# Optimization experiments

Hardware: AMD Instinct MI355X
Metric: run time of the kernel (lower is better)

The kernel has to match this reference:

```python
import jax, jax.numpy as jnp
import numpy as np

N_U = 50000; N_I = 50000; DIM = 64; NNZ = 2_000_000; Q = 5
LAYERS = 2; B = 1024; P = 10; NNEG = 40
MARGIN = 0.5; LAMBDA1 = 0.2; BATCH_USER = 1024


def setup_inputs() -> dict:
    key = jax.random.key(0)
    ks = jax.random.split(key, 12)
    return {
        "E_u_0": jax.random.normal(ks[0], (N_U, DIM), jnp.float32) * 0.1,
        "E_i_0": jax.random.normal(ks[1], (N_I, DIM), jnp.float32) * 0.1,
        "vals": jax.random.uniform(ks[2], (NNZ,), jnp.float32) * 0.05,  # normalized adj values
        "u_mul_s": jax.random.normal(ks[3], (N_U, Q), jnp.float32) * 0.1,
        "vt": jax.random.normal(ks[4], (Q, N_I), jnp.float32) * 0.1,
        "v_mul_s": jax.random.normal(ks[5], (N_I, Q), jnp.float32) * 0.1,
        "ut": jax.random.normal(ks[6], (Q, N_U), jnp.float32) * 0.1,
        "rows": jax.random.randint(ks[7], (NNZ,), 0, N_U, jnp.int32),
        "cols": jax.random.randint(ks[8], (NNZ,), 0, N_I, jnp.int32),
        "uids": jax.random.randint(ks[9], (B,), 0, N_U, jnp.int32),
        "pos": jax.random.randint(ks[10], (B, P), 0, N_I, jnp.int32),
        "neg": jax.random.randint(ks[11], (B, NNEG), 0, N_I, jnp.int32),
    }


def _leaky(x):
    return jnp.where(x > 0, x, 0.5 * x)  # LeakyReLU(0.5)


def reference(E_u_0, E_i_0, vals, u_mul_s, vt, v_mul_s, ut, rows, cols, uids, pos, neg):
    # --- GCN propagation (dropout=0 -> sparse_dropout is identity) ---
    E_u, E_i = E_u_0, E_i_0
    sum_u, sum_i = E_u_0, E_i_0
    for _ in range(LAYERS):
        # spmm(adj, E_i): out[r] += val * E_i[c]
        Z_du = _leaky(jax.ops.segment_sum(vals[:, None] * E_i[cols], rows, num_segments=N_U))
        # spmm(adj.T, E_u): out[c] += val * E_u[r]
        Z_di = _leaky(jax.ops.segment_sum(vals[:, None] * E_u[rows], cols, num_segments=N_I))
        # SVD hyper-conv (computed in original forward; unused by returned loss)
        G_u = _leaky(u_mul_s @ (vt @ E_i))
        G_i = _leaky(v_mul_s @ (ut @ E_u))
        del G_u, G_i
        E_u, E_i = Z_du + E_u, Z_di + E_i
        sum_u, sum_i = sum_u + E_u, sum_i + E_i

    # --- U_IConstLoss, vectorized over the original per-uid Python loop ---
    u_emb = sum_u[uids]                                  # [B, D]
    pos_emb = sum_i[pos]                                 # [B, P, D]
    neg_emb = sum_i[neg]                                 # [B, N, D]
    pos_scores = jnp.einsum("bd,bpd->bp", u_emb, pos_emb)
    neg_scores = jnp.einsum("bd,bnd->bn", u_emb, neg_emb)
    # pos_d = score at argmin == min; neg_d = score at argmax == max
    pos_d = pos_scores.min(axis=1)
    neg_d = neg_scores.max(axis=1)
    delta = jnp.where(neg_d - pos_d > 0.005, 10.0 * (pos_d - neg_d), 0.0)
    # loss_d accumulates across the loop and the running value is added each iter
    loss_d_cum = jnp.cumsum(delta)
    pos_hinge = jax.nn.relu(1.0 - pos_scores).sum(axis=1)          # sum over P
    neg_hinge = jax.nn.relu(neg_scores - MARGIN).sum(axis=1)       # scalar per user
    bpr_sum = pos_hinge + P * neg_hinge                            # bpr.sum() per user
    loss_r = (bpr_sum.sum() + loss_d_cum.sum()) / BATCH_USER
    loss = loss_r + LAMBDA1
    return loss
```

## Files before the change

### kernel.cpp

```cpp
#include <hip/hip_runtime.h>

#define N_U   50000
#define N_I   50000
#define NSEG  (N_U + N_I)
#define DIM   64
#define B_USERS 1024
#define P_POS 10
#define N_NEG 40

#define BSEG  128
#define NBUK  782
#define CAP   8192
#define EPB   4096
#define TPAD  16

#ifndef __has_builtin
#define __has_builtin(x) 0
#endif
#if __has_builtin(__builtin_amdgcn_cvt_pk_f32_fp8) && __has_builtin(__builtin_amdgcn_cvt_pk_fp8_f32)
#define HAVE_FP8 1
#else
#define HAVE_FP8 0
#endif

typedef float f32x2 __attribute__((ext_vector_type(2)));

__device__ __forceinline__ unsigned f2b(float f) {
    unsigned b = __float_as_uint(f);
    return (b + 0x7FFFu + ((b >> 16) & 1u)) >> 16;
}
__device__ __forceinline__ float b2f(unsigned u) {
    return __uint_as_float(u << 16);
}
__device__ __forceinline__ float blo(unsigned u) { return __uint_as_float(u << 16); }
__device__ __forceinline__ float bhi(unsigned u) { return __uint_as_float(u & 0xFFFF0000u); }

#if !HAVE_FP8
__device__ __forceinline__ float dec8(unsigned v) {
    unsigned s = (v >> 7) & 1u, ef = (v >> 3) & 0xFu, m = v & 7u;
    float r = (ef == 0u) ? (float)m * 0.001953125f
                         : __uint_as_float(((ef + 120u) << 23) | (m << 20));
    return s ? -r : r;
}
__device__ __forceinline__ unsigned enc8(float f) {
    unsigned b = __float_as_uint(f);
    unsigned s = b >> 31;
    float a = fabsf(f);
    if (a >= 448.f) return (s << 7) | 0x7Eu;
    if (a < 0.015625f) return s << 7;
    int e = (int)((b >> 23) & 0xFF) - 120;
    unsigned m = b & 0x7FFFFFu;
    unsigned keep = m >> 20, rem = m & 0xFFFFFu;
    keep += (rem > 0x80000u) || (rem == 0x80000u && (keep & 1u));
    if (keep == 8u) { keep = 0u; ++e; if (e > 15) return (s << 7) | 0x7Eu; }
    if (e == 15 && keep == 7u) keep = 6u;
    return (s << 7) | ((unsigned)e << 3) | keep;
}
#endif

__device__ __forceinline__ void dec4v(unsigned u, f32x2& p01, f32x2& p23) {
#if HAVE_FP8
    p01 = __builtin_amdgcn_cvt_pk_f32_fp8((int)u, false);
    p23 = __builtin_amdgcn_cvt_pk_f32_fp8((int)u, true);
#else
    p01.x = dec8(u & 0xFFu); p01.y = dec8((u >> 8) & 0xFFu);
    p23.x = dec8((u >> 16) & 0xFFu); p23.y = dec8(u >> 24);
#endif
}
__device__ __forceinline__ unsigned enc4(float f0, float f1, float f2, float f3) {
#if HAVE_FP8
    int w = 0;
    w = __builtin_amdgcn_cvt_pk_fp8_f32(f0, f1, w, false);
    w = __builtin_amdgcn_cvt_pk_fp8_f32(f2, f3, w, true);
    return (unsigned)w;
#else
    return enc8(f0) | (enc8(f1) << 8) | (enc8(f2) << 16) | (enc8(f3) << 24);
#endif
}

__device__ __forceinline__ void pkfma(f32x2& a, f32x2 b, f32x2 c) {
    asm("v_pk_fma_f32 %0, %1, %2, %0" : "+v"(a) : "v"(b), "v"(c));
}
__device__ __forceinline__ void pkadd(f32x2& a, f32x2 t) {
    asm("v_pk_add_f32 %0, %0, %1" : "+v"(a) : "v"(t));
}

__device__ __forceinline__ unsigned encv8(unsigned fbits) {
    unsigned exp8 = (fbits >> 23) & 0xFFu;
    unsigned man4 = ((fbits >> 19) & 0xFu) + ((fbits >> 18) & 1u);
    if (man4 == 16u) { man4 = 0u; exp8 += 1u; }
    int ex = (int)exp8 - 107;
    if (ex <= 0) return 0u;
    if (ex > 15) { ex = 15; man4 = 15u; }
    return ((unsigned)ex << 4) | man4;
}
__device__ __forceinline__ unsigned decv8(unsigned v8) {
    return v8 ? ((((v8 >> 4) + 107u) << 7) | ((v8 & 0xFu) << 3)) : 0u;
}

__global__ void k_conv(const float* __restrict__ Eu0, const float* __restrict__ Ei0,
                       ushort* __restrict__ E0b, unsigned* __restrict__ E0f8) {
    int p = blockIdx.x * blockDim.x + threadIdx.x;
    if (p >= NSEG * (DIM / 4)) return;
    float4 v = (p < N_U * (DIM / 4)) ? ((const float4*)Eu0)[p]
                                     : ((const float4*)Ei0)[p - N_U * (DIM / 4)];
    ushort4 o;
    o.x = (ushort)f2b(v.x); o.y = (ushort)f2b(v.y);
    o.z = (ushort)f2b(v.z); o.w = (ushort)f2b(v.w);
    ((ushort4*)E0b)[p] = o;
    E0f8[p] = enc4(v.x, v.y, v.z, v.w);
}

__global__ __launch_bounds__(512) void k_binA(const float* __restrict__ vals,
                                              const int* __restrict__ rows,
                                              const int* __restrict__ cols,
                                              int* __restrict__ tails,
                                              unsigned* __restrict__ stage, int nnz) {
    __shared__ int hist[1024];
    __shared__ int cur[NBUK];
    __shared__ int adj[NBUK];
    __shared__ uint2 srt[2 * EPB];
    int t = threadIdx.x;
    hist[t] = 0; hist[t + 512] = 0;
    __syncthreads();

    int e0 = blockIdx.x * EPB;
    int rem = nnz - e0;
    int ne = rem < EPB ? rem : EPB;
    int nrec = 2 * ne;

    for (int k = t; k < ne; k += 512) {
        int e = e0 + k;
        atomicAdd(&hist[rows[e] >> 7], 1);
        atomicAdd(&hist[(N_U + cols[e]) >> 7], 1);
    }
    __syncthreads();

    int v0 = hist[t], v1 = hist[t + 512];
    for (int o = 1; o < 1024; o <<= 1) {
        int x0 = (t >= o) ? hist[t - o] : 0;
        int x1 = (t + 512 >= o) ? hist[t + 512 - o] : 0;
        __syncthreads();
        hist[t] += x0; hist[t + 512] += x1;
        __syncthreads();
    }
    {
        int i0 = t, i1 = t + 512;
        int l0 = hist[i0] - v0, l1 = hist[i1] - v1;
        if (i0 < NBUK) {
            cur[i0] = l0;
            adj[i0] = (v0 ? atomicAdd(&tails[i0 * TPAD], v0) : 0) - l0;
        }
        if (i1 < NBUK) {
            cur[i1] = l1;
            adj[i1] = (v1 ? atomicAdd(&tails[i1 * TPAD], v1) : 0) - l1;
        }
    }
    __syncthreads();

    for (int k = t; k < ne; k += 512) {
        int e = e0 + k;
        int r = rows[e];
        int g = N_U + cols[e];
        unsigned v8 = encv8(__float_as_uint(vals[e]));
        int b0 = r >> 7;
        int rk0 = atomicAdd(&cur[b0], 1);
        uint2 s0; s0.x = (((unsigned)g) << 15) | (v8 << 7) | (unsigned)(r & 127);
        s0.y = (unsigned)b0;
        srt[rk0] = s0;
        int b1 = g >> 7;
        int rk1 = atomicAdd(&cur[b1], 1);
        uint2 s1; s1.x = (((unsigned)r) << 15) | (v8 << 7) | (unsigned)(g & 127);
        s1.y = (unsigned)b1;
        srt[rk1] = s1;
    }
    __syncthreads();

    for (int i = t; i < nrec; i += 512) {
        uint2 s = srt[i];
        int bkt = (int)s.y;
        int slot = i + adj[bkt];
        if (slot < CAP) stage[((size_t)bkt << 13) + slot] = s.x;
    }
}

__global__ __launch_bounds__(256) void k_binB2(const unsigned* __restrict__ stage,
                                               const int* __restrict__ tails,
                                               unsigned* __restrict__ edges,
                                               int* __restrict__ cnt,
                                               int* __restrict__ endo) {
    __shared__ int red[256];
    __shared__ int h[BSEG];
    __shared__ int sc[BSEG];
    __shared__ int cur[BSEG];
    int b = blockIdx.x, t = threadIdx.x;

    int part = 0;
    for (int i = t; i < b; i += 256) part += min(tails[i * TPAD], CAP);
    red[t] = part;
    __syncthreads();
    for (int o = 128; o > 0; o >>= 1) {
        if (t < o) red[t] += red[t + o];
        __syncthreads();
    }
    int bukoff_b = red[0];

    int cs = min(tails[b * TPAD], CAP);
    size_t sbase = (size_t)b << 13;
    if (t < BSEG) h[t] = 0;
    __syncthreads();
    for (int i = t; i < cs; i += 256)
        atomicAdd(&h[stage[sbase + i] & 127u], 1);
    __syncthreads();
    if (t < BSEG) sc[t] = h[t];
    __syncthreads();
    for (int o = 1; o < BSEG; o <<= 1) {
        int x = (t < BSEG && t >= o) ? sc[t - o] : 0;
        __syncthreads();
        if (t < BSEG) sc[t] += x;
        __syncthreads();
    }
    int seg0 = b * BSEG;
    if (t < BSEG) {
        int start = bukoff_b + sc[t] - h[t];
        cur[t] = start;
        int seg = seg0 + t;
        if (seg < NSEG) { cnt[seg] = h[t]; endo[seg] = start + h[t]; }
    }
    __syncthreads();
    for (int i = t; i < cs; i += 256) {
        unsigned rec = stage[sbase + i];
        int pos = atomicAdd(&cur[rec & 127u], 1);
        edges[pos] = (rec & 0xFFFF8000u) | decv8((rec >> 7) & 0xFFu);
    }
}

template <int WF8>
__global__ __launch_bounds__(256) void k_prop(const unsigned* __restrict__ edges,
                                              const int* __restrict__ endo,
                                              const int* __restrict__ cnt,
                                              const ushort* __restrict__ Ecur,
                                              const unsigned* __restrict__ F8cur,
                                              ushort* __restrict__ Enext,
                                              unsigned* __restrict__ F8next) {
    int sid  = (blockIdx.x * blockDim.x + threadIdx.x) >> 5;
    int lane = threadIdx.x & 63;
    if (sid >= NSEG) return;
    int l32  = lane & 31;
    int hbase = lane & 32;
    int qq   = l32 >> 3;
    int l7   = lane & 7;
    int end = endo[sid], n = cnt[sid], start = end - n;

    f32x2 a0 = {0.f, 0.f}, a1 = {0.f, 0.f}, a2 = {0.f, 0.f}, a3 = {0.f, 0.f};
    int b = 0;
    for (; b + 32 <= n; b += 32) {
        unsigned pk = edges[start + b + l32];
        #pragma unroll
        for (int j = 0; j < 32; j += 4) {
            unsigned pj = __shfl(pk, hbase + j + qq, 64);
            float v = __uint_as_float((pj & 0x7FFFu) << 16);
            unsigned idx = pj >> 15;
            uint2 ev = *(const uint2*)(F8cur + (size_t)idx * 16 + l7 * 2);
            f32x2 e01, e23, e45, e67;
            dec4v(ev.x, e01, e23);
            dec4v(ev.y, e45, e67);
            f32x2 vv = {v, v};
            pkfma(a0, vv, e01);
            pkfma(a1, vv, e23);
            pkfma(a2, vv, e45);
            pkfma(a3, vv, e67);
        }
    }
    if (b < n) {
        int k = b + l32;
        unsigned pk = (k < n) ? edges[start + k] : 0u;
        int m = n - b;
        #pragma unroll 2
        for (int j = 0; j < m; j += 4) {
            unsigned pj = __shfl(pk, hbase + j + qq, 64);
            float v = __uint_as_float((pj & 0x7FFFu) << 16);
            unsigned idx = pj >> 15;
            uint2 ev = *(const uint2*)(F8cur + (size_t)idx * 16 + l7 * 2);
            f32x2 e01, e23, e45, e67;
            dec4v(ev.x, e01, e23);
            dec4v(ev.y, e45, e67);
            f32x2 vv = {v, v};
            pkfma(a0, vv, e01);
            pkfma(a1, vv, e23);
            pkfma(a2, vv, e45);
            pkfma(a3, vv, e67);
        }
    }
    #pragma unroll
    for (int off = 8; off <= 16; off <<= 1) {
        f32x2 t;
        t.x = __shfl_xor(a0.x, off, 64); t.y = __shfl_xor(a0.y, off, 64); pkadd(a0, t);
        t.x = __shfl_xor(a1.x, off, 64); t.y = __shfl_xor(a1.y, off, 64); pkadd(a1, t);
        t.x = __shfl_xor(a2.x, off, 64); t.y = __shfl_xor(a2.y, off, 64); pkadd(a2, t);
        t.x = __shfl_xor(a3.x, off, 64); t.y = __shfl_xor(a3.y, off, 64); pkadd(a3, t);
    }
    if (qq == 0) {
        uint4 ec = ((const uint4*)(Ecur + (size_t)sid * DIM))[l7];
        float r0 = blo(ec.x) + (a0.x > 0.f ? a0.x : 0.5f * a0.x);
        float r1 = bhi(ec.x) + (a0.y > 0.f ? a0.y : 0.5f * a0.y);
        float r2 = blo(ec.y) + (a1.x > 0.f ? a1.x : 0.5f * a1.x);
        float r3 = bhi(ec.y) + (a1.y > 0.f ? a1.y : 0.5f * a1.y);
        float r4 = blo(ec.z) + (a2.x > 0.f ? a2.x : 0.5f * a2.x);
        float r5 = bhi(ec.z) + (a2.y > 0.f ? a2.y : 0.5f * a2.y);
        float r6 = blo(ec.w) + (a3.x > 0.f ? a3.x : 0.5f * a3.x);
        float r7 = bhi(ec.w) + (a3.y > 0.f ? a3.y : 0.5f * a3.y);
        uint4 o;
        o.x = f2b(r0) | (f2b(r1) << 16);
        o.y = f2b(r2) | (f2b(r3) << 16);
        o.z = f2b(r4) | (f2b(r5) << 16);
        o.w = f2b(r6) | (f2b(r7) << 16);
        ((uint4*)(Enext + (size_t)sid * DIM))[l7] = o;
        if (WF8) {
            uint2 st;
            st.x = enc4(r0, r1, r2, r3);
            st.y = enc4(r4, r5, r6, r7);
            *(uint2*)(F8next + (size_t)sid * 16 + l7 * 2) = st;
        }
    }
}

__global__ __launch_bounds__(256) void k_loss(const ushort* __restrict__ E0,
                                              const ushort* __restrict__ E1,
                                              const ushort* __restrict__ E2,
                                              const int* __restrict__ uids,
                                              const int* __restrict__ pos,
                                              const int* __restrict__ neg,
                                              float* __restrict__ acc,
                                              int* __restrict__ done,
                                              float* __restrict__ out) {
    int wid  = (blockIdx.x * blockDim.x + threadIdx.x) >> 6;
    int lane = threadIdx.x & 63;
    if (wid < B_USERS) {
        int uid = uids[wid];
        size_t ub = (size_t)uid * DIM + lane;
        float u = b2f(E0[ub]) + b2f(E1[ub]) + b2f(E2[ub]);

        float pos_min = 1e30f, pos_h = 0.0f;
        for (int p = 0; p < P_POS; ++p) {
            int it = pos[wid * P_POS + p];
            size_t ib = (size_t)(N_U + it) * DIM + lane;
            float si = b2f(E0[ib]) + b2f(E1[ib]) + b2f(E2[ib]);
            float s = u * si;
            #pragma unroll
            for (int o = 32; o > 0; o >>= 1) s += __shfl_xor(s, o, 64);
            pos_min = fminf(pos_min, s);
            pos_h  += fmaxf(1.0f - s, 0.0f);
        }

        float neg_max = -1e30f, neg_h = 0.0f;
        for (int nn = 0; nn < N_NEG; ++nn) {
            int it = neg[wid * N_NEG + nn];
            size_t ib = (size_t)(N_U + it) * DIM + lane;
            float si = b2f(E0[ib]) + b2f(E1[ib]) + b2f(E2[ib]);
            float s = u * si;
            #pragma unroll
            for (int o = 32; o > 0; o >>= 1) s += __shfl_xor(s, o, 64);
            neg_max = fmaxf(neg_max, s);
            neg_h  += fmaxf(s - 0.5f, 0.0f);
        }

        float delta = (neg_max - pos_min > 0.005f) ? 10.0f * (pos_min - neg_max) : 0.0f;
        float contrib = pos_h + (float)P_POS * neg_h + delta * (float)(B_USERS - wid);
        if (lane == 0) atomicAdd(acc, contrib);
    }
    __syncthreads();
    if (threadIdx.x == 0) {
        __threadfence();
        int old = atomicAdd(done, 1);
        if (old == (int)gridDim.x - 1) {
            float a = atomicAdd(acc, 0.0f);
            out[0] = a / (float)B_USERS + 0.2f;
        }
    }
}

extern "C" void kernel_launch(void* const* d_in, const int* in_sizes, int n_in,
                              void* d_out, int out_size, void* d_ws, size_t ws_size,
                              hipStream_t stream) {
    const float* Eu0  = (const float*)d_in[0];
    const float* Ei0  = (const float*)d_in[1];
    const float* vals = (const float*)d_in[2];
    const int* rows = (const int*)d_in[7];
    const int* cols = (const int*)d_in[8];
    const int* uids = (const int*)d_in[9];
    const int* pos  = (const int*)d_in[10];
    const int* neg  = (const int*)d_in[11];
    int nnz = in_sizes[2];

    unsigned* edges  = (unsigned*)d_ws;
    unsigned* stage  = edges + (size_t)2 * nnz;
    ushort*   E0b    = (ushort*)(stage + (size_t)NBUK * CAP);
    ushort*   E1b    = E0b + (size_t)NSEG * DIM;
    ushort*   E2b    = E1b + (size_t)NSEG * DIM;
    unsigned* E0f8   = (unsigned*)(E2b + (size_t)NSEG * DIM);
    unsigned* E1f8   = E0f8 + (size_t)NSEG * 16;
    int*      cnt    = (int*)(E1f8 + (size_t)NSEG * 16);
    int*      endo   = cnt + NSEG;
    int*      tails  = endo + NSEG;
    float*    acc    = (float*)(tails + NBUK * TPAD);
    int*      done   = (int*)(acc + 1);

    const int blk = 256;

    hipMemsetAsync(tails, 0, (NBUK * TPAD + 2) * sizeof(int), stream);

    k_conv<<<(NSEG * (DIM / 4) + blk - 1) / blk, blk, 0, stream>>>(Eu0, Ei0, E0b, E0f8);
    k_binA<<<(nnz + EPB - 1) / EPB, 512, 0, stream>>>(vals, rows, cols, tails, stage, nnz);
    k_binB2<<<NBUK, blk, 0, stream>>>(stage, tails, edges, cnt, endo);

    const int prop_blocks = (NSEG * 32 + blk - 1) / blk;
    k_prop<1><<<prop_blocks, blk, 0, stream>>>(edges, endo, cnt, E0b, E0f8, E1b, E1f8);
    k_prop<0><<<prop_blocks, blk, 0, stream>>>(edges, endo, cnt, E1b, E1f8, E2b, nullptr);

    k_loss<<<(B_USERS * 64) / blk, blk, 0, stream>>>(E0b, E1b, E2b, uids, pos, neg,
                                                     acc, done, (float*)d_out);
}
```

Measured before the change: 198.9 us.

## Stripe bucket tail counters across blocks and precompute bucket offsets in separate scan

```diff
diff --git a/kernel.cpp b/kernel.cpp
--- a/kernel.cpp
+++ b/kernel.cpp
@@ -11,6 +11,8 @@
 #define BSEG  128
 #define NBUK  782
 #define CAP   8192
+#define NSTR  8
+#define SCAP  1024
 #define EPB   4096
 #define TPAD  16
 
@@ -121,6 +123,7 @@
     __shared__ int adj[NBUK];
     __shared__ uint2 srt[2 * EPB];
     int t = threadIdx.x;
+    int stripe = blockIdx.x & (NSTR - 1);
     hist[t] = 0; hist[t + 512] = 0;
     __syncthreads();
 
@@ -149,11 +152,11 @@
         int l0 = hist[i0] - v0, l1 = hist[i1] - v1;
         if (i0 < NBUK) {
             cur[i0] = l0;
-            adj[i0] = (v0 ? atomicAdd(&tails[i0 * TPAD], v0) : 0) - l0;
+            adj[i0] = (v0 ? atomicAdd(&tails[(i0 * NSTR + stripe) * TPAD], v0) : 0) - l0;
         }
         if (i1 < NBUK) {
             cur[i1] = l1;
-            adj[i1] = (v1 ? atomicAdd(&tails[i1 * TPAD], v1) : 0) - l1;
+            adj[i1] = (v1 ? atomicAdd(&tails[(i1 * NSTR + stripe) * TPAD], v1) : 0) - l1;
         }
     }
     __syncthreads();
@@ -180,37 +183,55 @@
         uint2 s = srt[i];
         int bkt = (int)s.y;
         int slot = i + adj[bkt];
-        if (slot < CAP) stage[((size_t)bkt << 13) + slot] = s.x;
-    }
+        if (slot < SCAP)
+            stage[((size_t)bkt << 13) + (stripe << 10) + slot] = s.x;
+    }
+}
+
+__global__ __launch_bounds__(1024) void k_bscan(const int* __restrict__ tails,
+                                                int* __restrict__ bukoff) {
+    __shared__ int sh[1024];
+    int t = threadIdx.x;
+    int v = 0;
+    if (t < NBUK) {
+        #pragma unroll
+        for (int s = 0; s < NSTR; ++s)
+            v += min(tails[(t * NSTR + s) * TPAD], SCAP);
+    }
+    sh[t] = v;
+    __syncthreads();
+    for (int o = 1; o < 1024; o <<= 1) {
+        int x = (t >= o) ? sh[t - o] : 0;
+        __syncthreads();
+        sh[t] += x;
+        __syncthreads();
+    }
+    if (t < NBUK) bukoff[t] = sh[t] - v;
 }
 
 __global__ __launch_bounds__(256) void k_binB2(const unsigned* __restrict__ stage,
                                                const int* __restrict__ tails,
+                                               const int* __restrict__ bukoff,
                                                unsigned* __restrict__ edges,
                                                int* __restrict__ cnt,
                                                int* __restrict__ endo) {
-    __shared__ int red[256];
     __shared__ int h[BSEG];
     __shared__ int sc[BSEG];
     __shared__ int cur[BSEG];
+    __shared__ int cs[NSTR];
     int b = blockIdx.x, t = threadIdx.x;
-
-    int part = 0;
-    for (int i = t; i < b; i += 256) part += min(tails[i * TPAD], CAP);
-    red[t] = part;
-    __syncthreads();
-    for (int o = 128; o > 0; o >>= 1) {
-        if (t < o) red[t] += red[t + o];
-        __syncthreads();
-    }
-    int bukoff_b = red[0];
-
-    int cs = min(tails[b * TPAD], CAP);
+    if (t < NSTR) cs[t] = min(tails[(b * NSTR + t) * TPAD], SCAP);
+    if (t < BSEG) h[t] = 0;
+    __syncthreads();
+
     size_t sbase = (size_t)b << 13;
-    if (t < BSEG) h[t] = 0;
-    __syncthreads();
-    for (int i = t; i < cs; i += 256)
-        atomicAdd(&h[stage[sbase + i] & 127u], 1);
+    #pragma unroll
+    for (int s = 0; s < NSTR; ++s) {
+        int c = cs[s];
+        const unsigned* w = stage + sbase + (s << 10);
+        for (int i = t; i < c; i += 256)
+            atomicAdd(&h[w[i] & 127u], 1);
+    }
     __syncthreads();
     if (t < BSEG) sc[t] = h[t];
     __syncthreads();
@@ -221,6 +242,7 @@
         __syncthreads();
     }
     int seg0 = b * BSEG;
+    int bukoff_b = bukoff[b];
     if (t < BSEG) {
         int start = bukoff_b + sc[t] - h[t];
         cur[t] = start;
@@ -228,10 +250,15 @@
         if (seg < NSEG) { cnt[seg] = h[t]; endo[seg] = start + h[t]; }
     }
     __syncthreads();
-    for (int i = t; i < cs; i += 256) {
-        unsigned rec = stage[sbase + i];
-        int pos = atomicAdd(&cur[rec & 127u], 1);
-        edges[pos] = (rec & 0xFFFF8000u) | decv8((rec >> 7) & 0xFFu);
+    #pragma unroll
+    for (int s = 0; s < NSTR; ++s) {
+        int c = cs[s];
+        const unsigned* w = stage + sbase + (s << 10);
+        for (int i = t; i < c; i += 256) {
+            unsigned rec = w[i];
+            int pos = atomicAdd(&cur[rec & 127u], 1);
+            edges[pos] = (rec & 0xFFFF8000u) | decv8((rec >> 7) & 0xFFu);
+        }
     }
 }
 
@@ -402,17 +429,19 @@
     unsigned* E1f8   = E0f8 + (size_t)NSEG * 16;
     int*      cnt    = (int*)(E1f8 + (size_t)NSEG * 16);
     int*      endo   = cnt + NSEG;
-    int*      tails  = endo + NSEG;
-    float*    acc    = (float*)(tails + NBUK * TPAD);
+    int*      bukoff = endo + NSEG;
+    int*      tails  = bukoff + NBUK;
+    float*    acc    = (float*)(tails + NBUK * NSTR * TPAD);
     int*      done   = (int*)(acc + 1);
 
     const int blk = 256;
 
-    hipMemsetAsync(tails, 0, (NBUK * TPAD + 2) * sizeof(int), stream);
+    hipMemsetAsync(tails, 0, ((size_t)NBUK * NSTR * TPAD + 2) * sizeof(int), stream);
 
     k_conv<<<(NSEG * (DIM / 4) + blk - 1) / blk, blk, 0, stream>>>(Eu0, Ei0, E0b, E0f8);
     k_binA<<<(nnz + EPB - 1) / EPB, 512, 0, stream>>>(vals, rows, cols, tails, stage, nnz);
-    k_binB2<<<NBUK, blk, 0, stream>>>(stage, tails, edges, cnt, endo);
+    k_bscan<<<1, 1024, 0, stream>>>(tails, bukoff);
+    k_binB2<<<NBUK, blk, 0, stream>>>(stage, tails, bukoff, edges, cnt, endo);
 
     const int prop_blocks = (NSEG * 32 + blk - 1) / blk;
     k_prop<1><<<prop_blocks, blk, 0, stream>>>(edges, endo, cnt, E0b, E0f8, E1b, E1f8);
```

New measurement: 200.0 us. About the same (+0.6%).
